# Performance work log

Hardware: AMD Instinct MI355X
Metric: run time of the kernel (lower is better)

The kernel has to match this reference:

```python
import jax, jax.numpy as jnp
import numpy as np

NUM_HEADS = 16


def setup_inputs() -> dict:
    key = jax.random.key(0)
    ks = jax.random.split(key, 5)
    B, S, D = 2, 2048, 1024
    scale = 0.02
    return {
        "x": jax.random.normal(ks[0], (B, S, D), dtype=jnp.float32),
        "Wq": jax.random.normal(ks[1], (D, D), dtype=jnp.float32) * scale,
        "Wk": jax.random.normal(ks[2], (D, D), dtype=jnp.float32) * scale,
        "Wv": jax.random.normal(ks[3], (D, D), dtype=jnp.float32) * scale,
        "Wo": jax.random.normal(ks[4], (D, D), dtype=jnp.float32) * scale,
        "bo": jnp.zeros((D,), dtype=jnp.float32),
    }


def reference(x, Wq, Wk, Wv, Wo, bo):
    B, S, D = x.shape
    H = NUM_HEADS
    Dh = D // H
    # project and split heads -> [B, H, S, Dh]
    q = (x @ Wq).reshape(B, S, H, Dh).transpose(0, 2, 1, 3)
    k = (x @ Wk).reshape(B, S, H, Dh).transpose(0, 2, 1, 3)
    v = (x @ Wv).reshape(B, S, H, Dh).transpose(0, 2, 1, 3)
    # full causal attention scores [B, H, S, S]
    scores = jnp.einsum("bhqd,bhkd->bhqk", q, k)
    causal_mask = jnp.triu(jnp.ones((S, S), dtype=bool), k=1)
    scores = jnp.where(causal_mask, -jnp.inf, scores)
    attn = jax.nn.softmax(scores / jnp.sqrt(jnp.float32(Dh)), axis=-1)
    ctx = jnp.einsum("bhqk,bhkd->bhqd", attn, v)
    ctx = ctx.transpose(0, 2, 1, 3).reshape(B, S, D)
    return ctx @ Wo + bo
```

## Files before the change

kernel.cpp:

```cpp
#include <hip/hip_runtime.h>
#include <hip/hip_bf16.h>
#include <math.h>

typedef __bf16 bf16_t;
typedef bf16_t bf16x4 __attribute__((ext_vector_type(4)));
typedef bf16_t bf16x8 __attribute__((ext_vector_type(8)));
typedef float f32x4 __attribute__((ext_vector_type(4)));

#define MFMA16(a, b, c) __builtin_amdgcn_mfma_f32_16x16x32_bf16(a, b, c, 0, 0, 0)
#define NEG_BIG (-1e30f)

__global__ __launch_bounds__(256) void cvt_bf16(const float* __restrict__ in,
                                                bf16_t* __restrict__ out, int n) {
    int i = (blockIdx.x * 256 + threadIdx.x) * 4;
    if (i < n) {
        float4 v = *(const float4*)(in + i);
        out[i + 0] = (bf16_t)v.x;
        out[i + 1] = (bf16_t)v.y;
        out[i + 2] = (bf16_t)v.z;
        out[i + 3] = (bf16_t)v.w;
    }
}

__global__ __launch_bounds__(256) void transpose_w(const float* __restrict__ W,
                                                   bf16_t* __restrict__ WT) {
    __shared__ float tile[32][33];
    int bx = blockIdx.x * 32, by = blockIdx.y * 32;
    int tx = threadIdx.x, ty = threadIdx.y;
    for (int i = 0; i < 32; i += 8)
        tile[ty + i][tx] = W[(size_t)(by + ty + i) * 1024 + bx + tx];
    __syncthreads();
    for (int i = 0; i < 32; i += 8)
        WT[(size_t)(bx + ty + i) * 1024 + by + tx] = (bf16_t)tile[tx][ty + i];
}

__global__ __launch_bounds__(256) void gemm_qkv(const bf16_t* __restrict__ X,
                                                const bf16_t* __restrict__ WT,
                                                bf16_t* __restrict__ Qd,
                                                bf16_t* __restrict__ Kd,
                                                bf16_t* __restrict__ Vd) {
    __shared__ bf16_t Asm[128][72];
    __shared__ bf16_t Bsm[128][72];
    const int which = blockIdx.z;
    const bf16_t* Wt = WT + (size_t)which * 1024 * 1024;
    const int bm = blockIdx.y * 128;
    const int bn = blockIdx.x * 128;
    const int tid = threadIdx.x;
    const int wave = tid >> 6, lane = tid & 63;
    const int wm = (wave >> 1) * 64, wn = (wave & 1) * 64;
    const int col = lane & 15, quad = lane >> 4;
    const int lrow = tid >> 1;
    const int lcol = (tid & 1) * 32;

    f32x4 acc[4][4] = {};

    for (int k0 = 0; k0 < 1024; k0 += 64) {
        const bf16_t* ga = X + (size_t)(bm + lrow) * 1024 + k0 + lcol;
        const bf16_t* gb = Wt + (size_t)(bn + lrow) * 1024 + k0 + lcol;
        *(bf16x8*)&Asm[lrow][lcol]      = *(const bf16x8*)ga;
        *(bf16x8*)&Asm[lrow][lcol + 8]  = *(const bf16x8*)(ga + 8);
        *(bf16x8*)&Asm[lrow][lcol + 16] = *(const bf16x8*)(ga + 16);
        *(bf16x8*)&Asm[lrow][lcol + 24] = *(const bf16x8*)(ga + 24);
        *(bf16x8*)&Bsm[lrow][lcol]      = *(const bf16x8*)gb;
        *(bf16x8*)&Bsm[lrow][lcol + 8]  = *(const bf16x8*)(gb + 8);
        *(bf16x8*)&Bsm[lrow][lcol + 16] = *(const bf16x8*)(gb + 16);
        *(bf16x8*)&Bsm[lrow][lcol + 24] = *(const bf16x8*)(gb + 24);
        __syncthreads();
        for (int ks = 0; ks < 2; ks++) {
            bf16x8 af[4], bfr[4];
            for (int mi = 0; mi < 4; mi++)
                af[mi] = *(const bf16x8*)&Asm[wm + mi * 16 + col][ks * 32 + quad * 8];
            for (int ni = 0; ni < 4; ni++)
                bfr[ni] = *(const bf16x8*)&Bsm[wn + ni * 16 + col][ks * 32 + quad * 8];
            for (int mi = 0; mi < 4; mi++)
                for (int ni = 0; ni < 4; ni++)
                    acc[mi][ni] = MFMA16(af[mi], bfr[ni], acc[mi][ni]);
        }
        __syncthreads();
    }

    for (int mi = 0; mi < 4; mi++) {
        for (int ni = 0; ni < 4; ni++) {
            int mbase = bm + wm + mi * 16 + quad * 4;
            int n = bn + wn + ni * 16 + col;
            int h = n >> 6, dh = n & 63;
            for (int r = 0; r < 4; r++) {
                int m = mbase + r;
                int b = m >> 11, s = m & 2047;
                size_t bh = (size_t)b * 16 + h;
                bf16_t val = (bf16_t)acc[mi][ni][r];
                if (which == 0)      Qd[(bh * 2048 + s) * 64 + dh] = val;
                else if (which == 1) Kd[(bh * 2048 + s) * 64 + dh] = val;
                else                 Vd[(bh * 64 + dh) * 2048 + s] = val;
            }
        }
    }
}

#define SD 72
__global__ __launch_bounds__(256) void attn(const bf16_t* __restrict__ Q,
                                            const bf16_t* __restrict__ K,
                                            const bf16_t* __restrict__ VT,
                                            bf16_t* __restrict__ CTX) {
    __shared__ bf16_t Ks[2][64][SD];
    __shared__ bf16_t Vs[2][64][SD];
    __shared__ bf16_t Ps[4][16][SD];

    const int bh = blockIdx.y;
    const int pr = blockIdx.x;
    const int tid = threadIdx.x;
    const int wave = tid >> 6, lane = tid & 63;
    const int col = lane & 15, quad = lane >> 4;

    const bf16_t* Qb = Q + (size_t)bh * 2048 * 64;
    const bf16_t* Kb = K + (size_t)bh * 2048 * 64;
    const bf16_t* Vb = VT + (size_t)bh * 64 * 2048;

    const int srow = tid >> 2;
    const int sseg = (tid & 3) * 16;

    const int b_ = bh >> 4, h_ = bh & 15;

    int g = 0;
    for (int ph = 0; ph < 2; ph++) {
        const int qt = ph ? (31 - pr) : pr;
        const int q0 = qt * 64;

        const int qrow = q0 + wave * 16 + col;
        const bf16x8 qf0 = *(const bf16x8*)&Qb[(size_t)qrow * 64 + quad * 8];
        const bf16x8 qf1 = *(const bf16x8*)&Qb[(size_t)qrow * 64 + 32 + quad * 8];

        f32x4 o[4] = {};
        float lsum = 0.f;

        const int nt = qt + 1;
        for (int t = 0; t < nt; t++, g++) {
            const int bsel = g & 1;
            const int k0 = t * 64;
            const bf16_t* gk = &Kb[(size_t)(k0 + srow) * 64 + sseg];
            *(bf16x8*)&Ks[bsel][srow][sseg]     = *(const bf16x8*)gk;
            *(bf16x8*)&Ks[bsel][srow][sseg + 8] = *(const bf16x8*)(gk + 8);
            const bf16_t* gv = &Vb[(size_t)srow * 2048 + k0 + sseg];
            *(bf16x8*)&Vs[bsel][srow][sseg]     = *(const bf16x8*)gv;
            *(bf16x8*)&Vs[bsel][srow][sseg + 8] = *(const bf16x8*)(gv + 8);
            __syncthreads();

            const bool diag = (t == qt);
            for (int ksub = 0; ksub < 4; ksub++) {
                bf16x8 a0 = *(const bf16x8*)&Ks[bsel][ksub * 16 + col][quad * 8];
                bf16x8 a1 = *(const bf16x8*)&Ks[bsel][ksub * 16 + col][32 + quad * 8];
                f32x4 z = {};
                z = MFMA16(a0, qf0, z);
                z = MFMA16(a1, qf1, z);
                if (diag) {
                    for (int r = 0; r < 4; r++) {
                        int lk = ksub * 16 + quad * 4 + r;
                        if (lk > wave * 16 + col) z[r] = NEG_BIG;
                    }
                }
                bf16x4 pw;
                for (int r = 0; r < 4; r++) {
                    float p = __expf(z[r] * 0.125f);
                    lsum += p;
                    pw[r] = (bf16_t)p;
                }
                *(bf16x4*)&Ps[wave][col][ksub * 16 + quad * 4] = pw;
            }

            for (int ck = 0; ck < 2; ck++) {
                bf16x8 pf = *(const bf16x8*)&Ps[wave][col][ck * 32 + quad * 8];
                for (int d = 0; d < 4; d++) {
                    bf16x8 vf = *(const bf16x8*)&Vs[bsel][d * 16 + col][ck * 32 + quad * 8];
                    o[d] = MFMA16(pf, vf, o[d]);
                }
            }
        }

        float lt = lsum + __shfl_xor(lsum, 16, 64);
        lt += __shfl_xor(lt, 32, 64);
        float lq[4];
        for (int r = 0; r < 4; r++)
            lq[r] = __shfl(lt, quad * 4 + r, 64);

        for (int d = 0; d < 4; d++) {
            for (int r = 0; r < 4; r++) {
                int s = q0 + wave * 16 + quad * 4 + r;
                int dh = d * 16 + col;
                CTX[((size_t)(b_ * 2048 + s)) * 1024 + h_ * 64 + dh] =
                    (bf16_t)(o[d][r] / fmaxf(lq[r], 1e-20f));
            }
        }
        __syncthreads();
    }
}

__global__ __launch_bounds__(256) void gemm_out(const bf16_t* __restrict__ X,
                                                const bf16_t* __restrict__ WT,
                                                const float* __restrict__ BO,
                                                float* __restrict__ OUT) {
    __shared__ bf16_t Asm[128][72];
    __shared__ bf16_t Bsm[128][72];
    const int bm = blockIdx.y * 128;
    const int bn = blockIdx.x * 128;
    const int tid = threadIdx.x;
    const int wave = tid >> 6, lane = tid & 63;
    const int wm = (wave >> 1) * 64, wn = (wave & 1) * 64;
    const int col = lane & 15, quad = lane >> 4;
    const int lrow = tid >> 1;
    const int lcol = (tid & 1) * 32;

    f32x4 acc[4][4] = {};

    for (int k0 = 0; k0 < 1024; k0 += 64) {
        const bf16_t* ga = X + (size_t)(bm + lrow) * 1024 + k0 + lcol;
        const bf16_t* gb = WT + (size_t)(bn + lrow) * 1024 + k0 + lcol;
        *(bf16x8*)&Asm[lrow][lcol]      = *(const bf16x8*)ga;
        *(bf16x8*)&Asm[lrow][lcol + 8]  = *(const bf16x8*)(ga + 8);
        *(bf16x8*)&Asm[lrow][lcol + 16] = *(const bf16x8*)(ga + 16);
        *(bf16x8*)&Asm[lrow][lcol + 24] = *(const bf16x8*)(ga + 24);
        *(bf16x8*)&Bsm[lrow][lcol]      = *(const bf16x8*)gb;
        *(bf16x8*)&Bsm[lrow][lcol + 8]  = *(const bf16x8*)(gb + 8);
        *(bf16x8*)&Bsm[lrow][lcol + 16] = *(const bf16x8*)(gb + 16);
        *(bf16x8*)&Bsm[lrow][lcol + 24] = *(const bf16x8*)(gb + 24);
        __syncthreads();
        for (int ks = 0; ks < 2; ks++) {
            bf16x8 af[4], bfr[4];
            for (int mi = 0; mi < 4; mi++)
                af[mi] = *(const bf16x8*)&Asm[wm + mi * 16 + col][ks * 32 + quad * 8];
            for (int ni = 0; ni < 4; ni++)
                bfr[ni] = *(const bf16x8*)&Bsm[wn + ni * 16 + col][ks * 32 + quad * 8];
            for (int mi = 0; mi < 4; mi++)
                for (int ni = 0; ni < 4; ni++)
                    acc[mi][ni] = MFMA16(af[mi], bfr[ni], acc[mi][ni]);
        }
        __syncthreads();
    }

    for (int mi = 0; mi < 4; mi++) {
        for (int ni = 0; ni < 4; ni++) {
            int mbase = bm + wm + mi * 16 + quad * 4;
            int n = bn + wn + ni * 16 + col;
            float bov = BO[n];
            for (int r = 0; r < 4; r++) {
                int m = mbase + r;
                OUT[(size_t)m * 1024 + n] = acc[mi][ni][r] + bov;
            }
        }
    }
}

extern "C" void kernel_launch(void* const* d_in, const int* in_sizes, int n_in,
                              void* d_out, int out_size, void* d_ws, size_t ws_size,
                              hipStream_t stream) {
    const float* x  = (const float*)d_in[0];
    const float* Wq = (const float*)d_in[1];
    const float* Wk = (const float*)d_in[2];
    const float* Wv = (const float*)d_in[3];
    const float* Wo = (const float*)d_in[4];
    const float* bo = (const float*)d_in[5];
    float* out = (float*)d_out;

    const size_t MEG = 1048576;
    bf16_t* base  = (bf16_t*)d_ws;
    bf16_t* Xb    = base;
    bf16_t* WTqkv = base + 4 * MEG;
    bf16_t* WoT   = base + 7 * MEG;
    bf16_t* Qb    = base + 8 * MEG;
    bf16_t* Kb    = base + 12 * MEG;
    bf16_t* Vb    = base + 16 * MEG;
    bf16_t* Cb    = base + 20 * MEG;

    cvt_bf16<<<4096, 256, 0, stream>>>(x, Xb, 4 * MEG);

    dim3 tb(32, 8);
    transpose_w<<<dim3(32, 32), tb, 0, stream>>>(Wq, WTqkv);
    transpose_w<<<dim3(32, 32), tb, 0, stream>>>(Wk, WTqkv + 1 * MEG);
    transpose_w<<<dim3(32, 32), tb, 0, stream>>>(Wv, WTqkv + 2 * MEG);
    transpose_w<<<dim3(32, 32), tb, 0, stream>>>(Wo, WoT);

    gemm_qkv<<<dim3(8, 32, 3), 256, 0, stream>>>(Xb, WTqkv, Qb, Kb, Vb);
    attn<<<dim3(16, 32), 256, 0, stream>>>(Qb, Kb, Vb, Cb);
    gemm_out<<<dim3(8, 32), 256, 0, stream>>>(Cb, WoT, bo, out);
}
```

Measured before the change: 205.7 us.

## Use direct global-to-LDS loads with XOR swizzle in GEMMs and attention

Replaces the register-staged global-to-shared copies in the QKV GEMM, attention and output GEMM with direct global_load_lds transfers into unpadded tiles that use an XOR swizzle, so LDS reads stay free of bank conflicts. The QKV GEMM swaps the MFMA operand order for V so the transposed V store writes contiguous sequence positions. The output GEMM is retiled to 64-row blocks, doubling the grid for better occupancy. This removes VGPR staging and padding but relies on the swizzle and per-wave load mapping being exactly right.

```diff
diff --git a/kernel.cpp b/kernel.cpp
--- a/kernel.cpp
+++ b/kernel.cpp
@@ -9,6 +9,12 @@
 
 #define MFMA16(a, b, c) __builtin_amdgcn_mfma_f32_16x16x32_bf16(a, b, c, 0, 0, 0)
 #define NEG_BIG (-1e30f)
+
+#define GLL16(gp, lp)                                                          \
+    __builtin_amdgcn_global_load_lds(                                          \
+        (const __attribute__((address_space(1))) unsigned int*)(gp),           \
+        (__attribute__((address_space(3))) unsigned int*)(lp), 16, 0, 0)
+
 
 __global__ __launch_bounds__(256) void cvt_bf16(const float* __restrict__ in,
                                                 bf16_t* __restrict__ out, int n) {
@@ -39,8 +45,8 @@
                                                 bf16_t* __restrict__ Qd,
                                                 bf16_t* __restrict__ Kd,
                                                 bf16_t* __restrict__ Vd) {
-    __shared__ bf16_t Asm[128][72];
-    __shared__ bf16_t Bsm[128][72];
+    __shared__ bf16_t AsmF[128 * 64];
+    __shared__ bf16_t BsmF[128 * 64];
     const int which = blockIdx.z;
     const bf16_t* Wt = WT + (size_t)which * 1024 * 1024;
     const int bm = blockIdx.y * 128;
@@ -49,75 +55,103 @@
     const int wave = tid >> 6, lane = tid & 63;
     const int wm = (wave >> 1) * 64, wn = (wave & 1) * 64;
     const int col = lane & 15, quad = lane >> 4;
-    const int lrow = tid >> 1;
-    const int lcol = (tid & 1) * 32;
+    const int cswz = col & 7;
+    const int lr8 = lane >> 3;
+    const int jg = (lane & 7) ^ lr8;
+
+    const int srow = wave * 32 + lr8;
+    const bf16_t* gA = X  + (size_t)(bm + srow) * 1024 + jg * 8;
+    const bf16_t* gB = Wt + (size_t)(bn + srow) * 1024 + jg * 8;
+    bf16_t* lA = AsmF + wave * 2048;
+    bf16_t* lB = BsmF + wave * 2048;
 
     f32x4 acc[4][4] = {};
 
     for (int k0 = 0; k0 < 1024; k0 += 64) {
-        const bf16_t* ga = X + (size_t)(bm + lrow) * 1024 + k0 + lcol;
-        const bf16_t* gb = Wt + (size_t)(bn + lrow) * 1024 + k0 + lcol;
-        *(bf16x8*)&Asm[lrow][lcol]      = *(const bf16x8*)ga;
-        *(bf16x8*)&Asm[lrow][lcol + 8]  = *(const bf16x8*)(ga + 8);
-        *(bf16x8*)&Asm[lrow][lcol + 16] = *(const bf16x8*)(ga + 16);
-        *(bf16x8*)&Asm[lrow][lcol + 24] = *(const bf16x8*)(ga + 24);
-        *(bf16x8*)&Bsm[lrow][lcol]      = *(const bf16x8*)gb;
-        *(bf16x8*)&Bsm[lrow][lcol + 8]  = *(const bf16x8*)(gb + 8);
-        *(bf16x8*)&Bsm[lrow][lcol + 16] = *(const bf16x8*)(gb + 16);
-        *(bf16x8*)&Bsm[lrow][lcol + 24] = *(const bf16x8*)(gb + 24);
+        for (int j = 0; j < 4; j++) {
+            GLL16(gA + (size_t)j * 8192 + k0, lA + j * 512);
+            GLL16(gB + (size_t)j * 8192 + k0, lB + j * 512);
+        }
         __syncthreads();
         for (int ks = 0; ks < 2; ks++) {
             bf16x8 af[4], bfr[4];
             for (int mi = 0; mi < 4; mi++)
-                af[mi] = *(const bf16x8*)&Asm[wm + mi * 16 + col][ks * 32 + quad * 8];
+                af[mi] = *(const bf16x8*)&AsmF[(wm + mi * 16 + col) * 64 +
+                                               (((ks << 2) + quad) ^ cswz) * 8];
             for (int ni = 0; ni < 4; ni++)
-                bfr[ni] = *(const bf16x8*)&Bsm[wn + ni * 16 + col][ks * 32 + quad * 8];
-            for (int mi = 0; mi < 4; mi++)
-                for (int ni = 0; ni < 4; ni++)
-                    acc[mi][ni] = MFMA16(af[mi], bfr[ni], acc[mi][ni]);
-        }
-        __syncthreads();
-    }
-
-    for (int mi = 0; mi < 4; mi++) {
-        for (int ni = 0; ni < 4; ni++) {
-            int mbase = bm + wm + mi * 16 + quad * 4;
-            int n = bn + wn + ni * 16 + col;
-            int h = n >> 6, dh = n & 63;
-            for (int r = 0; r < 4; r++) {
-                int m = mbase + r;
+                bfr[ni] = *(const bf16x8*)&BsmF[(wn + ni * 16 + col) * 64 +
+                                                (((ks << 2) + quad) ^ cswz) * 8];
+            if (which != 2) {
+                for (int mi = 0; mi < 4; mi++)
+                    for (int ni = 0; ni < 4; ni++)
+                        acc[mi][ni] = MFMA16(af[mi], bfr[ni], acc[mi][ni]);
+            } else {
+                for (int mi = 0; mi < 4; mi++)
+                    for (int ni = 0; ni < 4; ni++)
+                        acc[mi][ni] = MFMA16(bfr[ni], af[mi], acc[mi][ni]);
+            }
+        }
+        __syncthreads();
+    }
+
+    if (which != 2) {
+        for (int mi = 0; mi < 4; mi++) {
+            for (int ni = 0; ni < 4; ni++) {
+                int mbase = bm + wm + mi * 16 + quad * 4;
+                int n = bn + wn + ni * 16 + col;
+                int h = n >> 6, dh = n & 63;
+                for (int r = 0; r < 4; r++) {
+                    int m = mbase + r;
+                    int b = m >> 11, s = m & 2047;
+                    size_t bh = (size_t)b * 16 + h;
+                    bf16_t val = (bf16_t)acc[mi][ni][r];
+                    if (which == 0) Qd[(bh * 2048 + s) * 64 + dh] = val;
+                    else            Kd[(bh * 2048 + s) * 64 + dh] = val;
+                }
+            }
+        }
+    } else {
+        for (int mi = 0; mi < 4; mi++) {
+            for (int ni = 0; ni < 4; ni++) {
+                int nbase = bn + wn + ni * 16 + quad * 4;
+                int m = bm + wm + mi * 16 + col;
                 int b = m >> 11, s = m & 2047;
-                size_t bh = (size_t)b * 16 + h;
-                bf16_t val = (bf16_t)acc[mi][ni][r];
-                if (which == 0)      Qd[(bh * 2048 + s) * 64 + dh] = val;
-                else if (which == 1) Kd[(bh * 2048 + s) * 64 + dh] = val;
-                else                 Vd[(bh * 64 + dh) * 2048 + s] = val;
-            }
-        }
-    }
-}
-
-#define SD 72
+                for (int r = 0; r < 4; r++) {
+                    int n = nbase + r;
+                    int h = n >> 6, dh = n & 63;
+                    size_t bh = (size_t)b * 16 + h;
+                    Vd[(bh * 64 + dh) * 2048 + s] = (bf16_t)acc[mi][ni][r];
+                }
+            }
+        }
+    }
+}
+
+#define PSD 72
 __global__ __launch_bounds__(256) void attn(const bf16_t* __restrict__ Q,
                                             const bf16_t* __restrict__ K,
                                             const bf16_t* __restrict__ VT,
                                             bf16_t* __restrict__ CTX) {
-    __shared__ bf16_t Ks[2][64][SD];
-    __shared__ bf16_t Vs[2][64][SD];
-    __shared__ bf16_t Ps[4][16][SD];
+    __shared__ bf16_t KsF[2 * 64 * 64];
+    __shared__ bf16_t VsF[2 * 64 * 64];
+    __shared__ bf16_t Ps[4][16][PSD];
 
     const int bh = blockIdx.y;
     const int pr = blockIdx.x;
     const int tid = threadIdx.x;
     const int wave = tid >> 6, lane = tid & 63;
     const int col = lane & 15, quad = lane >> 4;
+    const int cswz = col & 7;
+    const int lr8 = lane >> 3;
+    const int jg = (lane & 7) ^ lr8;
 
     const bf16_t* Qb = Q + (size_t)bh * 2048 * 64;
     const bf16_t* Kb = K + (size_t)bh * 2048 * 64;
     const bf16_t* Vb = VT + (size_t)bh * 64 * 2048;
 
-    const int srow = tid >> 2;
-    const int sseg = (tid & 3) * 16;
+    const int strow = wave * 16 + lr8;
+    const bf16_t* gK = Kb + (size_t)strow * 64 + jg * 8;
+    const bf16_t* gV = Vb + (size_t)strow * 2048 + jg * 8;
 
     const int b_ = bh >> 4, h_ = bh & 15;
 
@@ -137,18 +171,22 @@
         for (int t = 0; t < nt; t++, g++) {
             const int bsel = g & 1;
             const int k0 = t * 64;
-            const bf16_t* gk = &Kb[(size_t)(k0 + srow) * 64 + sseg];
-            *(bf16x8*)&Ks[bsel][srow][sseg]     = *(const bf16x8*)gk;
-            *(bf16x8*)&Ks[bsel][srow][sseg + 8] = *(const bf16x8*)(gk + 8);
-            const bf16_t* gv = &Vb[(size_t)srow * 2048 + k0 + sseg];
-            *(bf16x8*)&Vs[bsel][srow][sseg]     = *(const bf16x8*)gv;
-            *(bf16x8*)&Vs[bsel][srow][sseg + 8] = *(const bf16x8*)(gv + 8);
+            bf16_t* lK = KsF + bsel * 4096 + wave * 1024;
+            bf16_t* lV = VsF + bsel * 4096 + wave * 1024;
+            for (int j = 0; j < 2; j++) {
+                GLL16(gK + (size_t)(k0 + j * 8) * 64, lK + j * 512);
+                GLL16(gV + (size_t)(k0 + j * 8 * 2048), lV + j * 512);
+            }
             __syncthreads();
 
             const bool diag = (t == qt);
+            const bf16_t* Kbuf = KsF + bsel * 4096;
+            const bf16_t* Vbuf = VsF + bsel * 4096;
             for (int ksub = 0; ksub < 4; ksub++) {
-                bf16x8 a0 = *(const bf16x8*)&Ks[bsel][ksub * 16 + col][quad * 8];
-                bf16x8 a1 = *(const bf16x8*)&Ks[bsel][ksub * 16 + col][32 + quad * 8];
+                bf16x8 a0 = *(const bf16x8*)&Kbuf[(ksub * 16 + col) * 64 +
+                                                  (quad ^ cswz) * 8];
+                bf16x8 a1 = *(const bf16x8*)&Kbuf[(ksub * 16 + col) * 64 +
+                                                  ((4 + quad) ^ cswz) * 8];
                 f32x4 z = {};
                 z = MFMA16(a0, qf0, z);
                 z = MFMA16(a1, qf1, z);
@@ -170,7 +208,8 @@
             for (int ck = 0; ck < 2; ck++) {
                 bf16x8 pf = *(const bf16x8*)&Ps[wave][col][ck * 32 + quad * 8];
                 for (int d = 0; d < 4; d++) {
-                    bf16x8 vf = *(const bf16x8*)&Vs[bsel][d * 16 + col][ck * 32 + quad * 8];
+                    bf16x8 vf = *(const bf16x8*)&Vbuf[(d * 16 + col) * 64 +
+                                                      (((ck << 2) + quad) ^ cswz) * 8];
                     o[d] = MFMA16(pf, vf, o[d]);
                 }
             }
@@ -198,45 +237,49 @@
                                                 const bf16_t* __restrict__ WT,
                                                 const float* __restrict__ BO,
                                                 float* __restrict__ OUT) {
-    __shared__ bf16_t Asm[128][72];
-    __shared__ bf16_t Bsm[128][72];
-    const int bm = blockIdx.y * 128;
+    __shared__ bf16_t AsmF[64 * 64];
+    __shared__ bf16_t BsmF[128 * 64];
+    const int bm = blockIdx.y * 64;
     const int bn = blockIdx.x * 128;
     const int tid = threadIdx.x;
     const int wave = tid >> 6, lane = tid & 63;
-    const int wm = (wave >> 1) * 64, wn = (wave & 1) * 64;
+    const int wm = (wave >> 1) * 32, wn = (wave & 1) * 64;
     const int col = lane & 15, quad = lane >> 4;
-    const int lrow = tid >> 1;
-    const int lcol = (tid & 1) * 32;
-
-    f32x4 acc[4][4] = {};
+    const int cswz = col & 7;
+    const int lr8 = lane >> 3;
+    const int jg = (lane & 7) ^ lr8;
+
+    const int arow = wave * 16 + lr8;
+    const int brow = wave * 32 + lr8;
+    const bf16_t* gA = X  + (size_t)(bm + arow) * 1024 + jg * 8;
+    const bf16_t* gB = WT + (size_t)(bn + brow) * 1024 + jg * 8;
+    bf16_t* lA = AsmF + wave * 1024;
+    bf16_t* lB = BsmF + wave * 2048;
+
+    f32x4 acc[2][4] = {};
 
     for (int k0 = 0; k0 < 1024; k0 += 64) {
-        const bf16_t* ga = X + (size_t)(bm + lrow) * 1024 + k0 + lcol;
-        const bf16_t* gb = WT + (size_t)(bn + lrow) * 1024 + k0 + lcol;
-        *(bf16x8*)&Asm[lrow][lcol]      = *(const bf16x8*)ga;
-        *(bf16x8*)&Asm[lrow][lcol + 8]  = *(const bf16x8*)(ga + 8);
-        *(bf16x8*)&Asm[lrow][lcol + 16] = *(const bf16x8*)(ga + 16);
-        *(bf16x8*)&Asm[lrow][lcol + 24] = *(const bf16x8*)(ga + 24);
-        *(bf16x8*)&Bsm[lrow][lcol]      = *(const bf16x8*)gb;
-        *(bf16x8*)&Bsm[lrow][lcol + 8]  = *(const bf16x8*)(gb + 8);
-        *(bf16x8*)&Bsm[lrow][lcol + 16] = *(const bf16x8*)(gb + 16);
-        *(bf16x8*)&Bsm[lrow][lcol + 24] = *(const bf16x8*)(gb + 24);
+        for (int j = 0; j < 2; j++)
+            GLL16(gA + (size_t)j * 8192 + k0, lA + j * 512);
+        for (int j = 0; j < 4; j++)
+            GLL16(gB + (size_t)j * 8192 + k0, lB + j * 512);
         __syncthreads();
         for (int ks = 0; ks < 2; ks++) {
-            bf16x8 af[4], bfr[4];
-            for (int mi = 0; mi < 4; mi++)
-                af[mi] = *(const bf16x8*)&Asm[wm + mi * 16 + col][ks * 32 + quad * 8];
+            bf16x8 af[2], bfr[4];
+            for (int mi = 0; mi < 2; mi++)
+                af[mi] = *(const bf16x8*)&AsmF[(wm + mi * 16 + col) * 64 +
+                                               (((ks << 2) + quad) ^ cswz) * 8];
             for (int ni = 0; ni < 4; ni++)
-                bfr[ni] = *(const bf16x8*)&Bsm[wn + ni * 16 + col][ks * 32 + quad * 8];
-            for (int mi = 0; mi < 4; mi++)
+                bfr[ni] = *(const bf16x8*)&BsmF[(wn + ni * 16 + col) * 64 +
+                                                (((ks << 2) + quad) ^ cswz) * 8];
+            for (int mi = 0; mi < 2; mi++)
                 for (int ni = 0; ni < 4; ni++)
                     acc[mi][ni] = MFMA16(af[mi], bfr[ni], acc[mi][ni]);
         }
         __syncthreads();
     }
 
-    for (int mi = 0; mi < 4; mi++) {
+    for (int mi = 0; mi < 2; mi++) {
         for (int ni = 0; ni < 4; ni++) {
             int mbase = bm + wm + mi * 16 + quad * 4;
             int n = bn + wn + ni * 16 + col;
@@ -280,5 +323,5 @@
 
     gemm_qkv<<<dim3(8, 32, 3), 256, 0, stream>>>(Xb, WTqkv, Qb, Kb, Vb);
     attn<<<dim3(16, 32), 256, 0, stream>>>(Qb, Kb, Vb, Cb);
-    gemm_out<<<dim3(8, 32), 256, 0, stream>>>(Cb, WoT, bo, out);
-}
+    gemm_out<<<dim3(8, 64), 256, 0, stream>>>(Cb, WoT, bo, out);
+}
```

Result: faster. 192.5 us (-6.4%).
